# Kernel tuning notes

Hardware: AMD Instinct MI355X
Metric: run time of the kernel (lower is better)

Reference implementation:

```python
import jax, jax.numpy as jnp
import numpy as np

WEIGHTS = {'seg': 1.0, 'grid': 0.5, 'baseline': 0.8, 'theta': 0.3, 'signal': 2.0}
IGNORE = 255


def _bce(p, t):
    # torch BCELoss: clamps log terms at -100
    lp = jnp.maximum(jnp.log(jnp.clip(p, 1e-12, 1.0)), -100.0)
    l1p = jnp.maximum(jnp.log(jnp.clip(1.0 - p, 1e-12, 1.0)), -100.0)
    return -(t * lp + (1.0 - t) * l1p).mean()


def _ce_ignore(logits, target):
    # logits (B,C,H,W), target (B,H,W) int; mean over target != 255
    logp = jax.nn.log_softmax(logits, axis=1)
    valid = target != IGNORE
    t_safe = jnp.where(valid, target, 0)
    nll = -jnp.take_along_axis(logp, t_safe[:, None].astype(jnp.int32), axis=1)[:, 0]
    return (nll * valid).sum() / jnp.maximum(valid.sum(), 1)


def _dice(logits, target, num_classes):
    p = jax.nn.softmax(logits, axis=1)                      # (B,C,H,W)
    oh = jax.nn.one_hot(target, num_classes, dtype=p.dtype) # (B,H,W,C)
    oh = jnp.transpose(oh, (0, 3, 1, 2))
    inter = (p * oh).sum(axis=(2, 3))
    union = p.sum(axis=(2, 3)) + oh.sum(axis=(2, 3))
    dice = (2.0 * inter + 1e-07) / (union + 1e-07)
    return 1.0 - dice.mean()


def _resize_bilinear_ac(x, out_h, out_w):
    # align_corners=True bilinear, x: (B,C,H,W)
    B, C, H, Wd = x.shape
    ys = jnp.linspace(0.0, H - 1.0, out_h)
    xs = jnp.linspace(0.0, Wd - 1.0, out_w)
    y0 = jnp.floor(ys).astype(jnp.int32); y1 = jnp.minimum(y0 + 1, H - 1); wy = (ys - y0).astype(x.dtype)
    x0 = jnp.floor(xs).astype(jnp.int32); x1 = jnp.minimum(x0 + 1, Wd - 1); wx = (xs - x0).astype(x.dtype)
    rows = x[:, :, y0, :] * (1 - wy)[None, None, :, None] + x[:, :, y1, :] * wy[None, None, :, None]
    out = rows[:, :, :, x0] * (1 - wx) + rows[:, :, :, x1] * wx
    return out


def _normalize_signal_masked(sig, mask):
    # sig, mask: (B,12,T); per-lead min/max normalize on valid region
    mf = mask.astype(sig.dtype)
    cnt = mf.sum(-1, keepdims=True)
    mn = jnp.min(jnp.where(mask, sig, jnp.inf), -1, keepdims=True)
    mx = jnp.max(jnp.where(mask, sig, -jnp.inf), -1, keepdims=True)
    rng = mx - mn
    ok = (cnt >= 2) & (rng >= 1e-06)
    mn_s = jnp.where(ok, mn, 0.0)
    rng_s = jnp.where(ok, rng, 1.0)
    norm = (2.0 * (sig - mn_s) / (rng_s + 1e-08) - 1.0) * mf
    return jnp.where(ok, norm, 0.0)


def _masked_mae(pred, target, mask):
    mf = mask.astype(pred.dtype)
    return (jnp.abs(pred - target) * mf).sum() / (mf.sum() + 1e-07)


def _masked_pearson(pred, target, mask):
    mf = mask.astype(pred.dtype)
    cnt = mf.sum(-1)                                   # (B,12)
    cs = jnp.maximum(cnt, 1.0)
    pm = (pred * mf).sum(-1) / cs
    tm = (target * mf).sum(-1) / cs
    pc = (pred - pm[..., None]) * mf
    tc = (target - tm[..., None]) * mf
    num = (pc * tc).sum(-1)
    ps = jnp.sqrt((pc ** 2).sum(-1) + 1e-06)
    ts = jnp.sqrt((tc ** 2).sum(-1) + 1e-06)
    corr = jnp.clip(num / (ps * ts + 1e-06), -1.0, 1.0)
    valid = (cnt >= 10).astype(pred.dtype)
    n_valid = valid.sum()
    avg = (corr * valid).sum() / jnp.maximum(n_valid, 1.0)
    return jnp.where(n_valid > 0, 1.0 - avg, 1.0)


def setup_inputs() -> dict:
    key = jax.random.key(0)
    ks = jax.random.split(key, 11)
    B, H, Wd, T = 8, 512, 512, 5000
    return {
        'wave_seg_pred': jax.random.normal(ks[0], (B, 13, H, Wd), jnp.float32),
        'wave_seg_target': jax.random.randint(ks[1], (B, H, Wd), 0, 13, jnp.int32),
        'grid_pred': jax.random.uniform(ks[2], (B, 1, H, Wd), jnp.float32),
        'grid_target': jax.random.uniform(ks[3], (B, 1, H, Wd), jnp.float32),
        'baseline_pred': jax.random.uniform(ks[4], (B, 12, H // 16, Wd // 16), jnp.float32),
        'baseline_target': jax.random.uniform(ks[5], (B, 12, H, Wd), jnp.float32),
        'theta_pred': jax.random.normal(ks[6], (B, 2, 3), jnp.float32),
        'theta_gt': jax.random.normal(ks[7], (B, 2, 3), jnp.float32),
        'signal_pred': jax.random.normal(ks[8], (B, 12, T), jnp.float32),
        'gt_signal': jax.random.normal(ks[9], (B, T, 12), jnp.float32),
        'signal_mask': jax.random.randint(ks[10], (B, T, 12), 0, 2, jnp.int32).astype(bool),
    }


def reference(wave_seg_pred, wave_seg_target, grid_pred, grid_target,
              baseline_pred, baseline_target, theta_pred, theta_gt,
              signal_pred, gt_signal, signal_mask):
    # seg
    seg = (_ce_ignore(wave_seg_pred, wave_seg_target)
           + _dice(wave_seg_pred, wave_seg_target, 13)) * WEIGHTS['seg']
    # grid
    inter = (grid_pred * grid_target).sum()
    union = grid_pred.sum() + grid_target.sum()
    grid = (_bce(grid_pred, grid_target)
            + (1.0 - (2.0 * inter + 1e-07) / (union + 1e-07))) * WEIGHTS['grid']
    # baseline
    Hp, Wp = baseline_pred.shape[2], baseline_pred.shape[3]
    bt = _resize_bilinear_ac(baseline_target, Hp, Wp)
    baseline = _bce(baseline_pred, bt) * WEIGHTS['baseline']
    # theta
    theta = jnp.abs(theta_pred - theta_gt).mean() * WEIGHTS['theta']
    # signal
    sig_t = jnp.swapaxes(gt_signal, 1, 2)     # (B,12,T)
    m = jnp.swapaxes(signal_mask, 1, 2)       # (B,12,T)
    pn = _normalize_signal_masked(signal_pred, m)
    tn = _normalize_signal_masked(sig_t, m)
    signal = (_masked_mae(pn, tn, m) + _masked_pearson(pn, tn, m)) * WEIGHTS['signal']
    total = seg + grid + baseline + theta + signal
    return jnp.stack([seg, grid, baseline, theta, signal, total])
```

## Files before the change

### kernel.cpp

```cpp
#include <hip/hip_runtime.h>
#include <math.h>

#define WS_SEG_NLL    0
#define WS_SEG_VALID  8
#define WS_INTER      16
#define WS_PSUM       120
#define WS_OHCNT      224
#define WS_GRID_BCE   328
#define WS_GRID_INTER 329
#define WS_GRID_PSUM  330
#define WS_GRID_TSUM  331
#define WS_BASE_BCE   332
#define WS_SIG_ABS    333
#define WS_SIG_CNT    334
#define WS_SIG_CORR   335
#define WS_SIG_NV     336
#define WS_MASK_FLAG  337
#define WS_DONE       338
#define WS_SIGSTATS   340
#define WS_FLOATS     820

#define SEG_NB   2048
#define GRID_NB  256
#define BASE_NB  384
#define SIGA_NB  96
#define TOTAL_NB (SEG_NB + GRID_NB + BASE_NB + SIGA_NB)

__device__ inline float wave_sum(float v) {
    #pragma unroll
    for (int o = 32; o > 0; o >>= 1) v += __shfl_down(v, o, 64);
    return v;
}

template <int OP>
__device__ inline float blk_red(float v, float* sb) {
    #pragma unroll
    for (int o = 32; o > 0; o >>= 1) {
        float u = __shfl_down(v, o, 64);
        v = (OP == 0) ? (v + u) : ((OP == 1) ? fminf(v, u) : fmaxf(v, u));
    }
    __syncthreads();
    if ((threadIdx.x & 63) == 0) sb[threadIdx.x >> 6] = v;
    __syncthreads();
    const int nw = blockDim.x >> 6;
    float r = sb[0];
    for (int w = 1; w < nw; w++) {
        float u = sb[w];
        r = (OP == 0) ? (r + u) : ((OP == 1) ? fminf(r, u) : fmaxf(r, u));
    }
    return r;
}

__device__ void seg_part(int sb_idx, const float2* __restrict__ pred2,
                         const int2* __restrict__ tgt2, float* __restrict__ ws) {
    const int b  = sb_idx >> 8;
    const int xb = sb_idx & 255;
    const int HW2 = 131072;
    const float2* predb = pred2 + (size_t)b * 13 * HW2;
    const int2*   tgtb  = tgt2 + (size_t)b * HW2;

    __shared__ float s_inter[13];
    __shared__ float s_psum[13];
    __shared__ int   s_cnt[13];
    __shared__ float s_nll;
    __shared__ int   s_nval;
    if (threadIdx.x < 13) { s_inter[threadIdx.x] = 0.f; s_psum[threadIdx.x] = 0.f; s_cnt[threadIdx.x] = 0; }
    if (threadIdx.x == 13) s_nll = 0.f;
    if (threadIdx.x == 14) s_nval = 0;
    __syncthreads();

    float psum[13];
    #pragma unroll
    for (int c = 0; c < 13; c++) psum[c] = 0.f;
    int cnt[13];
    #pragma unroll
    for (int c = 0; c < 13; c++) cnt[c] = 0;
    float nll = 0.f;
    int nval = 0;

    #pragma unroll
    for (int it = 0; it < 2; it++) {
        const int j = xb * 256 + threadIdx.x + it * 65536;
        float2 x2[13];
        #pragma unroll
        for (int c = 0; c < 13; c++) x2[c] = predb[c * HW2 + j];
        const int2 t2 = tgtb[j];
        #pragma unroll
        for (int k = 0; k < 2; k++) {
            const int t = (k == 0) ? t2.x : t2.y;
            float x[13];
            #pragma unroll
            for (int c = 0; c < 13; c++) x[c] = (k == 0) ? x2[c].x : x2[c].y;
            float m = x[0];
            #pragma unroll
            for (int c = 1; c < 13; c++) m = fmaxf(m, x[c]);
            float xt = x[0];
            #pragma unroll
            for (int c = 1; c < 13; c++) xt = (c == t) ? x[c] : xt;
            float se = 0.f;
            #pragma unroll
            for (int c = 0; c < 13; c++) { x[c] = __expf(x[c] - m); se += x[c]; }
            const float inv = __builtin_amdgcn_rcpf(se);
            #pragma unroll
            for (int c = 0; c < 13; c++) psum[c] += x[c] * inv;
            #pragma unroll
            for (int c = 0; c < 13; c++) cnt[c] += __popcll(__ballot(t == c));
            nval += __popcll(__ballot(t != 255));
            const bool valid = (t != 255);
            if ((unsigned)t < 13u) {
                const float pt = __expf(xt - m) * inv;
                atomicAdd(&s_inter[t], pt);
            }
            nll += valid ? (m + __logf(se) - xt) : 0.f;
        }
    }

    const bool lane0 = (threadIdx.x & 63) == 0;
    #pragma unroll
    for (int c = 0; c < 13; c++) {
        float a = wave_sum(psum[c]);
        if (lane0) atomicAdd(&s_psum[c], a);
    }
    { float a = wave_sum(nll); if (lane0) atomicAdd(&s_nll, a); }
    if (lane0) {
        #pragma unroll
        for (int c = 0; c < 13; c++) atomicAdd(&s_cnt[c], cnt[c]);
        atomicAdd(&s_nval, nval);
    }
    __syncthreads();
    if (threadIdx.x < 13) {
        atomicAdd(&ws[WS_PSUM  + b * 13 + threadIdx.x], s_psum[threadIdx.x]);
        atomicAdd(&ws[WS_INTER + b * 13 + threadIdx.x], s_inter[threadIdx.x]);
        atomicAdd(&ws[WS_OHCNT + b * 13 + threadIdx.x], (float)s_cnt[threadIdx.x]);
    }
    if (threadIdx.x == 64) atomicAdd(&ws[WS_SEG_NLL + b],   s_nll);
    if (threadIdx.x == 65) atomicAdd(&ws[WS_SEG_VALID + b], (float)s_nval);
}

__device__ void grid_part(int gb, const float4* __restrict__ gp,
                          const float4* __restrict__ gt, float* __restrict__ ws) {
    const int N4 = 2097152 / 4;
    float bce = 0.f, inter = 0.f, ps = 0.f, ts = 0.f;
    const int stride = GRID_NB * 256;
    for (int i = gb * 256 + threadIdx.x; i < N4; i += stride) {
        const float4 p4 = gp[i];
        const float4 t4 = gt[i];
        const float pa[4] = {p4.x, p4.y, p4.z, p4.w};
        const float ta[4] = {t4.x, t4.y, t4.z, t4.w};
        #pragma unroll
        for (int k = 0; k < 4; k++) {
            const float p = pa[k], t = ta[k];
            const float pc  = fminf(fmaxf(p, 1e-12f), 1.0f);
            const float qc  = fminf(fmaxf(1.f - p, 1e-12f), 1.0f);
            const float lp  = fmaxf(__logf(pc), -100.f);
            const float l1p = fmaxf(__logf(qc), -100.f);
            bce  -= t * lp + (1.f - t) * l1p;
            inter += p * t;
            ps += p;
            ts += t;
        }
    }
    __shared__ float s4[4];
    if (threadIdx.x < 4) s4[threadIdx.x] = 0.f;
    __syncthreads();
    const bool lane0 = (threadIdx.x & 63) == 0;
    { float a = wave_sum(bce);   if (lane0) atomicAdd(&s4[0], a); }
    { float a = wave_sum(inter); if (lane0) atomicAdd(&s4[1], a); }
    { float a = wave_sum(ps);    if (lane0) atomicAdd(&s4[2], a); }
    { float a = wave_sum(ts);    if (lane0) atomicAdd(&s4[3], a); }
    __syncthreads();
    if (threadIdx.x == 0) {
        atomicAdd(&ws[WS_GRID_BCE],   s4[0]);
        atomicAdd(&ws[WS_GRID_INTER], s4[1]);
        atomicAdd(&ws[WS_GRID_PSUM],  s4[2]);
        atomicAdd(&ws[WS_GRID_TSUM],  s4[3]);
    }
}

__device__ void base_part(int bb, const float* __restrict__ bp,
                          const float* __restrict__ bt, float* __restrict__ ws) {
    const int idx = bb * 256 + threadIdx.x;
    const int w  = idx & 31;
    const int h  = (idx >> 5) & 31;
    const int bc = idx >> 10;
    const float* img = bt + (size_t)bc * 262144;
    const float step = 511.0f / 31.0f;
    const float yy = h * step, xx = w * step;
    int y0 = (int)floorf(yy); int y1 = min(y0 + 1, 511); const float wy = yy - y0;
    int x0 = (int)floorf(xx); int x1 = min(x0 + 1, 511); const float wx = xx - x0;
    const float v00 = img[y0 * 512 + x0], v01 = img[y0 * 512 + x1];
    const float v10 = img[y1 * 512 + x0], v11 = img[y1 * 512 + x1];
    const float r0 = v00 * (1.f - wy) + v10 * wy;
    const float r1 = v01 * (1.f - wy) + v11 * wy;
    const float t  = r0 * (1.f - wx) + r1 * wx;
    const float p  = bp[idx];
    const float pc  = fminf(fmaxf(p, 1e-12f), 1.0f);
    const float qc  = fminf(fmaxf(1.f - p, 1e-12f), 1.0f);
    const float lp  = fmaxf(__logf(pc), -100.f);
    const float l1p = fmaxf(__logf(qc), -100.f);
    const float bce = -(t * lp + (1.f - t) * l1p);

    __shared__ float sb[4];
    const float s = blk_red<0>(bce, sb);
    if (threadIdx.x == 0) atomicAdd(&ws[WS_BASE_BCE], s);
}

__device__ void sigA_part(int sl, const float* __restrict__ sp,
                          const float* __restrict__ st, const void* __restrict__ mp,
                          float* __restrict__ ws) {
    const int T = 5000;
    const int b = sl / 12, l = sl % 12;
    const float* ps = sp + (size_t)(b * 12 + l) * T;
    const float* ts_base = st + (size_t)b * T * 12 + l;
    const int* mi = (const int*)mp;
    const unsigned char* mb = (const unsigned char*)mp;
    const size_t mbase = (size_t)b * T * 12 + l;

    __shared__ float sb[4];
    __shared__ int s_flag;
    if (threadIdx.x == 0) s_flag = 0;
    __syncthreads();
    int f = 0;
    for (int i = threadIdx.x; i < 3072; i += blockDim.x)
        if ((i & 3) && mb[i]) f = 1;
    if (__any(f) && (threadIdx.x & 63) == 0) atomicOr(&s_flag, 1);
    __syncthreads();
    const bool m32 = (s_flag == 0);

    float cnt = 0.f;
    float mnp = __builtin_inff(), mxp = -__builtin_inff();
    float mnt = __builtin_inff(), mxt = -__builtin_inff();
    for (int t = threadIdx.x; t < T; t += blockDim.x) {
        const bool m = m32 ? (mi[mbase + (size_t)t * 12] != 0)
                           : (mb[mbase + (size_t)t * 12] != 0);
        const float p  = ps[t];
        const float tv = ts_base[(size_t)t * 12];
        if (m) {
            cnt += 1.f;
            mnp = fminf(mnp, p);  mxp = fmaxf(mxp, p);
            mnt = fminf(mnt, tv); mxt = fmaxf(mxt, tv);
        }
    }
    cnt = blk_red<0>(cnt, sb);
    mnp = blk_red<1>(mnp, sb); mxp = blk_red<2>(mxp, sb);
    mnt = blk_red<1>(mnt, sb); mxt = blk_red<2>(mxt, sb);

    if (threadIdx.x == 0) {
        float* o = ws + WS_SIGSTATS + sl * 5;
        o[0] = cnt; o[1] = mnp; o[2] = mxp; o[3] = mnt; o[4] = mxt;
        if (sl == 0) ws[WS_MASK_FLAG] = m32 ? 1.0f : 0.0f;
    }
}

__global__ __launch_bounds__(256) void mega_kernel(
        const float2* __restrict__ seg_pred, const int2* __restrict__ seg_tgt,
        const float4* __restrict__ grid_pred, const float4* __restrict__ grid_tgt,
        const float* __restrict__ base_pred, const float* __restrict__ base_tgt,
        const float* __restrict__ sig_p, const float* __restrict__ sig_t,
        const void* __restrict__ maskp, float* __restrict__ ws) {
    const int bx = blockIdx.x;
    if (bx < SEG_NB) {
        seg_part(bx, seg_pred, seg_tgt, ws);
    } else if (bx < SEG_NB + GRID_NB) {
        grid_part(bx - SEG_NB, grid_pred, grid_tgt, ws);
    } else if (bx < SEG_NB + GRID_NB + BASE_NB) {
        base_part(bx - SEG_NB - GRID_NB, base_pred, base_tgt, ws);
    } else {
        sigA_part(bx - SEG_NB - GRID_NB - BASE_NB, sig_p, sig_t, maskp, ws);
    }
}

__global__ __launch_bounds__(256) void sigB_kernel(
        const float* __restrict__ sp, const float* __restrict__ st,
        const void* __restrict__ mp, const float* __restrict__ tp,
        const float* __restrict__ tg, float* __restrict__ ws,
        float* __restrict__ out) {
    const int T = 5000;
    const int sl = blockIdx.x;
    const int b = sl / 12, l = sl % 12;
    const float* ps = sp + (size_t)(b * 12 + l) * T;
    const float* ts_base = st + (size_t)b * T * 12 + l;
    const int* mi = (const int*)mp;
    const unsigned char* mb = (const unsigned char*)mp;
    const size_t mbase = (size_t)b * T * 12 + l;

    __shared__ float sb[4];
    const bool m32 = ws[WS_MASK_FLAG] > 0.5f;
    const float* stats = ws + WS_SIGSTATS + sl * 5;
    const float cnt = stats[0];
    const float mnp = stats[1], mxp = stats[2], mnt = stats[3], mxt = stats[4];

    const float rngp = mxp - mnp, rngt = mxt - mnt;
    const bool okp = (cnt >= 2.f) && (rngp >= 1e-6f);
    const bool okt = (cnt >= 2.f) && (rngt >= 1e-6f);
    const float mnp_s = okp ? mnp : 0.f, rp = okp ? rngp : 1.f;
    const float mnt_s = okt ? mnt : 0.f, rt = okt ? rngt : 1.f;
    const float invp = 2.f / (rp + 1e-8f), invt = 2.f / (rt + 1e-8f);

    float S_p = 0.f, S_t = 0.f, S_pt = 0.f, S_pp = 0.f, S_tt = 0.f, S_abs = 0.f;
    for (int t = threadIdx.x; t < T; t += blockDim.x) {
        const bool m = m32 ? (mi[mbase + (size_t)t * 12] != 0)
                           : (mb[mbase + (size_t)t * 12] != 0);
        const float p  = ps[t];
        const float tv = ts_base[(size_t)t * 12];
        const float pn = (m && okp) ? ((p  - mnp_s) * invp - 1.f) : 0.f;
        const float tn = (m && okt) ? ((tv - mnt_s) * invt - 1.f) : 0.f;
        S_p += pn; S_t += tn;
        S_pt += pn * tn; S_pp += pn * pn; S_tt += tn * tn;
        S_abs += m ? fabsf(pn - tn) : 0.f;
    }
    S_p  = blk_red<0>(S_p, sb);
    S_t  = blk_red<0>(S_t, sb);
    S_pt = blk_red<0>(S_pt, sb);
    S_pp = blk_red<0>(S_pp, sb);
    S_tt = blk_red<0>(S_tt, sb);
    S_abs = blk_red<0>(S_abs, sb);

    __shared__ int s_last;
    if (threadIdx.x == 0) {
        const float cs = fmaxf(cnt, 1.f);
        const float pm = S_p / cs, tm = S_t / cs;
        const float num = S_pt - pm * S_t - tm * S_p + pm * tm * cnt;
        const float psd = sqrtf(fmaxf(S_pp - 2.f * pm * S_p + pm * pm * cnt, 0.f) + 1e-6f);
        const float tsd = sqrtf(fmaxf(S_tt - 2.f * tm * S_t + tm * tm * cnt, 0.f) + 1e-6f);
        float corr = num / (psd * tsd + 1e-6f);
        corr = fminf(fmaxf(corr, -1.f), 1.f);
        const float valid = (cnt >= 10.f) ? 1.f : 0.f;
        atomicAdd(&ws[WS_SIG_ABS],  S_abs);
        atomicAdd(&ws[WS_SIG_CNT],  cnt);
        atomicAdd(&ws[WS_SIG_CORR], corr * valid);
        atomicAdd(&ws[WS_SIG_NV],   valid);
        __threadfence();
        const int old = atomicAdd((int*)(ws + WS_DONE), 1);
        s_last = (old == 95) ? 1 : 0;
    }
    __syncthreads();
    if (!s_last) return;

    __shared__ float s_d, s_nll, s_nv, s_th;
    if (threadIdx.x == 0) { s_d = 0.f; s_nll = 0.f; s_nv = 0.f; s_th = 0.f; }
    __syncthreads();
    const int t = threadIdx.x;
    float d = 0.f, nll = 0.f, nv = 0.f, th = 0.f;
    if (t < 104) {
        const float it = ws[WS_INTER + t], p = ws[WS_PSUM + t], oh = ws[WS_OHCNT + t];
        d = (2.f * it + 1e-7f) / (p + oh + 1e-7f);
    }
    if (t < 8) { nll = ws[WS_SEG_NLL + t]; nv = ws[WS_SEG_VALID + t]; }
    if (t < 48) th = fabsf(tp[t] - tg[t]);
    d = wave_sum(d); nll = wave_sum(nll); nv = wave_sum(nv); th = wave_sum(th);
    if ((t & 63) == 0) {
        atomicAdd(&s_d, d); atomicAdd(&s_nll, nll);
        atomicAdd(&s_nv, nv); atomicAdd(&s_th, th);
    }
    __syncthreads();
    if (t == 0) {
        const float ce = s_nll / fmaxf(s_nv, 1.f);
        const float seg = (ce + (1.f - s_d / 104.f)) * 1.0f;
        const float bce_g = ws[WS_GRID_BCE] / 2097152.f;
        const float gd = 1.f - (2.f * ws[WS_GRID_INTER] + 1e-7f) /
                               (ws[WS_GRID_PSUM] + ws[WS_GRID_TSUM] + 1e-7f);
        const float grid = (bce_g + gd) * 0.5f;
        const float base = (ws[WS_BASE_BCE] / 98304.f) * 0.8f;
        const float theta = (s_th / 48.f) * 0.3f;
        const float sabs = atomicAdd(&ws[WS_SIG_ABS],  0.f);
        const float scnt = atomicAdd(&ws[WS_SIG_CNT],  0.f);
        const float scor = atomicAdd(&ws[WS_SIG_CORR], 0.f);
        const float snv  = atomicAdd(&ws[WS_SIG_NV],   0.f);
        const float mae = sabs / (scnt + 1e-7f);
        const float pear = (snv > 0.f) ? (1.f - scor / fmaxf(snv, 1.f)) : 1.f;
        const float sig = (mae + pear) * 2.0f;
        const float total = seg + grid + base + theta + sig;
        out[0] = seg; out[1] = grid; out[2] = base; out[3] = theta; out[4] = sig;
        out[5] = total;
    }
}

extern "C" void kernel_launch(void* const* d_in, const int* in_sizes, int n_in,
                              void* d_out, int out_size, void* d_ws, size_t ws_size,
                              hipStream_t stream) {
    const float* seg_pred  = (const float*)d_in[0];
    const int*   seg_tgt   = (const int*)d_in[1];
    const float* grid_pred = (const float*)d_in[2];
    const float* grid_tgt  = (const float*)d_in[3];
    const float* base_pred = (const float*)d_in[4];
    const float* base_tgt  = (const float*)d_in[5];
    const float* theta_p   = (const float*)d_in[6];
    const float* theta_g   = (const float*)d_in[7];
    const float* sig_p     = (const float*)d_in[8];
    const float* sig_t     = (const float*)d_in[9];
    const void*  maskp     = d_in[10];
    float* ws  = (float*)d_ws;
    float* out = (float*)d_out;

    hipMemsetAsync(d_ws, 0, WS_FLOATS * sizeof(float), stream);
    mega_kernel<<<TOTAL_NB, 256, 0, stream>>>(
        (const float2*)seg_pred, (const int2*)seg_tgt,
        (const float4*)grid_pred, (const float4*)grid_tgt,
        base_pred, base_tgt, sig_p, sig_t, maskp, ws);
    sigB_kernel<<<96, 256, 0, stream>>>(sig_p, sig_t, maskp, theta_p, theta_g, ws, out);
}
```

Before: 304.8 us.

## Stage segmentation tiles into LDS via direct global-to-LDS loads with fewer blocks

The segmentation part now uses 512 persistent-style blocks, each looping over 8 tiles of 512 pixels. Each tile's 13 logit channels and target values are staged into shared memory with the direct global-to-LDS load builtin, then read back per pixel. Per-class counts now use shared-memory atomics on valid pixels instead of per-pixel wave ballots. The aim is to improve memory-level parallelism and cut ballot overhead, at the cost of a barrier per tile with no double buffering and more LDS atomics.

```diff
diff --git a/kernel.cpp b/kernel.cpp
--- a/kernel.cpp
+++ b/kernel.cpp
@@ -20,11 +20,14 @@
 #define WS_SIGSTATS   340
 #define WS_FLOATS     820
 
-#define SEG_NB   2048
+#define SEG_NB   512
 #define GRID_NB  256
 #define BASE_NB  384
 #define SIGA_NB  96
 #define TOTAL_NB (SEG_NB + GRID_NB + BASE_NB + SIGA_NB)
+
+#define AS_GLOBAL const __attribute__((address_space(1))) void*
+#define AS_LDS    __attribute__((address_space(3))) void*
 
 __device__ inline float wave_sum(float v) {
     #pragma unroll
@@ -51,46 +54,55 @@
     return r;
 }
 
-__device__ void seg_part(int sb_idx, const float2* __restrict__ pred2,
-                         const int2* __restrict__ tgt2, float* __restrict__ ws) {
-    const int b  = sb_idx >> 8;
-    const int xb = sb_idx & 255;
-    const int HW2 = 131072;
-    const float2* predb = pred2 + (size_t)b * 13 * HW2;
-    const int2*   tgtb  = tgt2 + (size_t)b * HW2;
-
+__device__ void seg_part(int sb_idx, const float* __restrict__ pred,
+                         const int* __restrict__ tgt, float* __restrict__ ws) {
+    const int b   = sb_idx >> 6;
+    const int c64 = sb_idx & 63;
+    const int HW  = 262144;
+    const float* predf = pred + (size_t)b * 13 * HW;
+    const int*   tgtb  = tgt + (size_t)b * HW;
+
+    __shared__ alignas(16) float s_tile[28 * 256];
+    int* s_tgt_i = (int*)&s_tile[26 * 256];
     __shared__ float s_inter[13];
     __shared__ float s_psum[13];
     __shared__ int   s_cnt[13];
     __shared__ float s_nll;
-    __shared__ int   s_nval;
+    __shared__ float s_nval;
     if (threadIdx.x < 13) { s_inter[threadIdx.x] = 0.f; s_psum[threadIdx.x] = 0.f; s_cnt[threadIdx.x] = 0; }
     if (threadIdx.x == 13) s_nll = 0.f;
-    if (threadIdx.x == 14) s_nval = 0;
-    __syncthreads();
+    if (threadIdx.x == 14) s_nval = 0.f;
+
+    const int lane = threadIdx.x & 63;
+    const int wv   = threadIdx.x >> 6;
 
     float psum[13];
     #pragma unroll
     for (int c = 0; c < 13; c++) psum[c] = 0.f;
-    int cnt[13];
-    #pragma unroll
-    for (int c = 0; c < 13; c++) cnt[c] = 0;
-    float nll = 0.f;
-    int nval = 0;
-
-    #pragma unroll
-    for (int it = 0; it < 2; it++) {
-        const int j = xb * 256 + threadIdx.x + it * 65536;
-        float2 x2[13];
+    float nll = 0.f, nval = 0.f;
+
+    #pragma unroll 1
+    for (int tile = 0; tile < 8; tile++) {
+        const int px0 = c64 * 4096 + tile * 512;
         #pragma unroll
-        for (int c = 0; c < 13; c++) x2[c] = predb[c * HW2 + j];
-        const int2 t2 = tgtb[j];
+        for (int i = 0; i < 7; i++) {
+            const int k = wv * 7 + i;
+            const float* g;
+            if (k < 26) g = predf + (size_t)(k >> 1) * HW + px0 + (k & 1) * 256;
+            else        g = (const float*)(tgtb + px0 + (k - 26) * 256);
+            g += lane * 4;
+            __builtin_amdgcn_global_load_lds((AS_GLOBAL)g,
+                                             (AS_LDS)&s_tile[k * 256], 16, 0, 0);
+        }
+        __syncthreads();
+
         #pragma unroll
-        for (int k = 0; k < 2; k++) {
-            const int t = (k == 0) ? t2.x : t2.y;
+        for (int kp = 0; kp < 2; kp++) {
+            const int p = threadIdx.x + kp * 256;
+            const int t = s_tgt_i[p];
             float x[13];
             #pragma unroll
-            for (int c = 0; c < 13; c++) x[c] = (k == 0) ? x2[c].x : x2[c].y;
+            for (int c = 0; c < 13; c++) x[c] = s_tile[c * 512 + p];
             float m = x[0];
             #pragma unroll
             for (int c = 1; c < 13; c++) m = fmaxf(m, x[c]);
@@ -103,30 +115,24 @@
             const float inv = __builtin_amdgcn_rcpf(se);
             #pragma unroll
             for (int c = 0; c < 13; c++) psum[c] += x[c] * inv;
-            #pragma unroll
-            for (int c = 0; c < 13; c++) cnt[c] += __popcll(__ballot(t == c));
-            nval += __popcll(__ballot(t != 255));
-            const bool valid = (t != 255);
             if ((unsigned)t < 13u) {
-                const float pt = __expf(xt - m) * inv;
-                atomicAdd(&s_inter[t], pt);
+                atomicAdd(&s_inter[t], __expf(xt - m) * inv);
+                atomicAdd(&s_cnt[t], 1);
+                nll  += m + __logf(se) - xt;
+                nval += 1.f;
             }
-            nll += valid ? (m + __logf(se) - xt) : 0.f;
         }
-    }
-
-    const bool lane0 = (threadIdx.x & 63) == 0;
+        if (tile < 7) __syncthreads();
+    }
+
+    const bool lane0 = (lane == 0);
     #pragma unroll
     for (int c = 0; c < 13; c++) {
         float a = wave_sum(psum[c]);
         if (lane0) atomicAdd(&s_psum[c], a);
     }
-    { float a = wave_sum(nll); if (lane0) atomicAdd(&s_nll, a); }
-    if (lane0) {
-        #pragma unroll
-        for (int c = 0; c < 13; c++) atomicAdd(&s_cnt[c], cnt[c]);
-        atomicAdd(&s_nval, nval);
-    }
+    { float a = wave_sum(nll);  if (lane0) atomicAdd(&s_nll, a); }
+    { float a = wave_sum(nval); if (lane0) atomicAdd(&s_nval, a); }
     __syncthreads();
     if (threadIdx.x < 13) {
         atomicAdd(&ws[WS_PSUM  + b * 13 + threadIdx.x], s_psum[threadIdx.x]);
@@ -134,7 +140,7 @@
         atomicAdd(&ws[WS_OHCNT + b * 13 + threadIdx.x], (float)s_cnt[threadIdx.x]);
     }
     if (threadIdx.x == 64) atomicAdd(&ws[WS_SEG_NLL + b],   s_nll);
-    if (threadIdx.x == 65) atomicAdd(&ws[WS_SEG_VALID + b], (float)s_nval);
+    if (threadIdx.x == 65) atomicAdd(&ws[WS_SEG_VALID + b], s_nval);
 }
 
 __device__ void grid_part(int gb, const float4* __restrict__ gp,
@@ -253,7 +259,7 @@
 }
 
 __global__ __launch_bounds__(256) void mega_kernel(
-        const float2* __restrict__ seg_pred, const int2* __restrict__ seg_tgt,
+        const float* __restrict__ seg_pred, const int* __restrict__ seg_tgt,
         const float4* __restrict__ grid_pred, const float4* __restrict__ grid_tgt,
         const float* __restrict__ base_pred, const float* __restrict__ base_tgt,
         const float* __restrict__ sig_p, const float* __restrict__ sig_t,
@@ -395,7 +401,7 @@
 
     hipMemsetAsync(d_ws, 0, WS_FLOATS * sizeof(float), stream);
     mega_kernel<<<TOTAL_NB, 256, 0, stream>>>(
-        (const float2*)seg_pred, (const int2*)seg_tgt,
+        seg_pred, seg_tgt,
         (const float4*)grid_pred, (const float4*)grid_tgt,
         base_pred, base_tgt, sig_p, sig_t, maskp, ws);
     sigB_kernel<<<96, 256, 0, stream>>>(sig_p, sig_t, maskp, theta_p, theta_g, ws, out);
```

Measured after the change: 288.3 us. -5.4%, faster.
